# Optimization experiments

Measured on AMD Instinct MI355X. Metric: run time of the kernel, lower is better.

The kernel has to match this reference:

```python
import jax, jax.numpy as jnp
import numpy as np

B, N, D, L = 16, 100, 1024, 2000


def setup_inputs() -> dict:
    key = jax.random.key(0)
    ks = jax.random.split(key, 9)
    s = 1.0 / np.sqrt(D)
    return {
        "feature": jax.random.normal(ks[0], (B, N, D), dtype=jnp.float32),
        "graph": jax.random.randint(ks[1], (B, N, N), 0, L),
        "W0": jax.random.normal(ks[2], (D, D), dtype=jnp.float32) * s,
        "W1": jax.random.normal(ks[3], (D, D), dtype=jnp.float32) * s,
        "bias": jax.random.uniform(ks[4], (L, D), dtype=jnp.float32, minval=-s, maxval=s),
        "dp_Wa": jax.random.normal(ks[5], (D, D), dtype=jnp.float32) * s,
        "dp_ba": jax.random.normal(ks[6], (D,), dtype=jnp.float32) * s,
        "dp_Wb": jax.random.normal(ks[7], (D, D), dtype=jnp.float32) * s,
        "dp_bb": jax.random.normal(ks[8], (D,), dtype=jnp.float32) * s,
        "get_alpha": 0,
    }


def reference(feature, graph, W0, W1, bias, dp_Wa, dp_ba, dp_Wb, dp_bb, get_alpha):
    # ---- DirectedGraphConv.conv ----
    adj = (graph != 0).astype(feature.dtype)                     # [B,N,N]
    out = feature + feature @ W0.T + feature @ W1.T              # [B,N,D]
    out = out + jnp.take(bias, graph, axis=0).sum(axis=2)        # label-embedding gather+sum over neighbors
    # ---- relation_alpha: DotProduct(feature, feature) ----
    a = feature @ dp_Wa.T + dp_ba                                # [B,N,D]
    b = feature @ dp_Wb.T + dp_bb                                # [B,N,D]
    alpha = jnp.einsum('bik,bjk->bij', a, b)                     # [B,N,N]
    alpha = jnp.maximum(alpha, 0.0)                              # alpha[alpha<0]=0
    alpha = jnp.einsum('bij,bjk->bik', adj, alpha)               # bmm(adj, alpha)
    alpha = jax.nn.softmax(alpha, axis=1)                        # Softmax(dim=1)
    out = jnp.einsum('bij,bjk->bik', alpha, out)                 # bmm(alpha, output)
    if get_alpha:
        return (out, alpha)
    return out
```

## Files before the change

kernel.cpp:

```cpp
#include <hip/hip_runtime.h>
#include <stdint.h>

#define B_   16
#define N_   100
#define D_   1024
#define L_   2000
#define M_   1600

#define RCAP 24
#define ZMAX 2400
#define TC   12

typedef __bf16 bf16x8 __attribute__((ext_vector_type(8)));
typedef float  f32x4  __attribute__((ext_vector_type(4)));

__device__ __forceinline__ void gl_lds16(const __bf16* g, __bf16* l) {
    __builtin_amdgcn_global_load_lds(
        (const __attribute__((address_space(1))) void*)g,
        (__attribute__((address_space(3))) void*)l, 16, 0, 0);
}


__global__ void __launch_bounds__(256)
k_prep(const float* __restrict__ f,
       const float* __restrict__ W0, const float* __restrict__ W1,
       const float* __restrict__ Wa, const float* __restrict__ Wb,
       const float* __restrict__ bias,
       __bf16* __restrict__ fb, __bf16* __restrict__ wcat, __bf16* __restrict__ biasB) {
    int i = blockIdx.x * 256 + threadIdx.x;
    union { __bf16 h[8]; uint4 u; } pk;
    if (i < 204800) {
        long base = (long)i * 8;
        const float4* p = (const float4*)(f + base);
        float4 x = p[0], y = p[1];
        pk.h[0]=(__bf16)x.x; pk.h[1]=(__bf16)x.y; pk.h[2]=(__bf16)x.z; pk.h[3]=(__bf16)x.w;
        pk.h[4]=(__bf16)y.x; pk.h[5]=(__bf16)y.y; pk.h[6]=(__bf16)y.z; pk.h[7]=(__bf16)y.w;
        ((uint4*)fb)[i] = pk.u;
    } else if (i < 598016) {
        int j = i - 204800;
        long base = (long)j * 8;
        long seg = base >> 20;
        long off = base & ((1l << 20) - 1);
        if (seg == 0) {
            const float4* p0 = (const float4*)(W0 + off);
            const float4* p1 = (const float4*)(W1 + off);
            float4 a0 = p0[0], a1 = p0[1], b0 = p1[0], b1 = p1[1];
            pk.h[0]=(__bf16)(a0.x+b0.x); pk.h[1]=(__bf16)(a0.y+b0.y);
            pk.h[2]=(__bf16)(a0.z+b0.z); pk.h[3]=(__bf16)(a0.w+b0.w);
            pk.h[4]=(__bf16)(a1.x+b1.x); pk.h[5]=(__bf16)(a1.y+b1.y);
            pk.h[6]=(__bf16)(a1.z+b1.z); pk.h[7]=(__bf16)(a1.w+b1.w);
        } else {
            const float* src = (seg == 1) ? Wa : Wb;
            const float4* p = (const float4*)(src + off);
            float4 x = p[0], y = p[1];
            pk.h[0]=(__bf16)x.x; pk.h[1]=(__bf16)x.y; pk.h[2]=(__bf16)x.z; pk.h[3]=(__bf16)x.w;
            pk.h[4]=(__bf16)y.x; pk.h[5]=(__bf16)y.y; pk.h[6]=(__bf16)y.z; pk.h[7]=(__bf16)y.w;
        }
        ((uint4*)wcat)[j] = pk.u;
    } else {
        int j = i - 598016;
        long base = (long)j * 8;
        const float4* p = (const float4*)(bias + base);
        float4 x = p[0], y = p[1];
        pk.h[0]=(__bf16)x.x; pk.h[1]=(__bf16)x.y; pk.h[2]=(__bf16)x.z; pk.h[3]=(__bf16)x.w;
        pk.h[4]=(__bf16)y.x; pk.h[5]=(__bf16)y.y; pk.h[6]=(__bf16)y.z; pk.h[7]=(__bf16)y.w;
        ((uint4*)biasB)[j] = pk.u;
    }
}


#define BM 64
#define BN 128
#define BK 64

__global__ void __launch_bounds__(256)
k_gemm(const __bf16* __restrict__ A, const __bf16* __restrict__ Bw,
       const float* __restrict__ feat, const float* __restrict__ ba,
       const float* __restrict__ bbias,
       float* __restrict__ out0, float* __restrict__ aB, float* __restrict__ bB) {
    __shared__ __align__(16) __bf16 As[BM * BK];
    __shared__ __align__(16) __bf16 Bs[BN * BK];
    int t = threadIdx.x;
    int bm = blockIdx.x, bn = blockIdx.y;
    int lane = t & 63, wave = t >> 6;
    int wr = wave & 1, wc = wave >> 1;
    int lrow = lane & 15, quad = lane >> 4;

    f32x4 acc[2][4] = {};
    const __bf16* Ag = A  + (long)(bm * BM) * D_;
    const __bf16* Bg = Bw + (long)(bn * BN) * D_;

    for (int k0 = 0; k0 < D_; k0 += BK) {
        #pragma unroll
        for (int pi = 0; pi < 2; ++pi) {
            int p = pi * 256 + t, row = p >> 3, c = (p & 7) ^ (row & 7);
            gl_lds16(Ag + (long)row * D_ + k0 + c * 8, As + p * 8);
        }
        #pragma unroll
        for (int pi = 0; pi < 4; ++pi) {
            int p = pi * 256 + t, row = p >> 3, c = (p & 7) ^ (row & 7);
            gl_lds16(Bg + (long)row * D_ + k0 + c * 8, Bs + p * 8);
        }
        __syncthreads();
        #pragma unroll
        for (int ks = 0; ks < 2; ++ks) {
            bf16x8 af[2], bf[4];
            #pragma unroll
            for (int i = 0; i < 2; ++i) {
                int r = wr * 32 + i * 16 + lrow;
                int slot = r * 8 + (((ks << 2) | quad) ^ (r & 7));
                af[i] = *(const bf16x8*)(As + slot * 8);
            }
            #pragma unroll
            for (int j = 0; j < 4; ++j) {
                int r = wc * 64 + j * 16 + lrow;
                int slot = r * 8 + (((ks << 2) | quad) ^ (r & 7));
                bf[j] = *(const bf16x8*)(Bs + slot * 8);
            }
            #pragma unroll
            for (int i = 0; i < 2; ++i)
                #pragma unroll
                for (int j = 0; j < 4; ++j)
                    acc[i][j] = __builtin_amdgcn_mfma_f32_16x16x32_bf16(af[i], bf[j], acc[i][j], 0, 0, 0);
        }
        __syncthreads();
    }

    int nbase = bn * BN;
    int seg = nbase >> 10;
    #pragma unroll
    for (int i = 0; i < 2; ++i) {
        int gm0 = bm * BM + wr * 32 + i * 16 + quad * 4;
        #pragma unroll
        for (int j = 0; j < 4; ++j) {
            int col = (nbase + wc * 64 + j * 16 + lrow) & 1023;
            #pragma unroll
            for (int r = 0; r < 4; ++r) {
                long m = gm0 + r;
                float v = acc[i][j][r];
                if (seg == 0)      out0[m * D_ + col] = v + feat[m * D_ + col];
                else if (seg == 1) aB[m * D_ + col]   = v + ba[col];
                else               bB[m * D_ + col]   = v + bbias[col];
            }
        }
    }
}


__global__ void __launch_bounds__(256)
k_ga(const int* __restrict__ graph, const __bf16* __restrict__ biasB,
     float* __restrict__ out0, const float* __restrict__ aB,
     const float* __restrict__ bB, float* __restrict__ wl, float* __restrict__ cwG) {
    __shared__ int rowCnt[N_], rowOff[N_], rowRank[N_];
    __shared__ int ndvS, totZS;
    __shared__ int zjL[ZMAX];
    __shared__ short prL[ZMAX];
    __shared__ float corrL[RCAP][4];
    __shared__ float wred[4][4];

    int t = threadIdx.x;
    if (blockIdx.x < 1600) {
        int bi = blockIdx.x;
        if (t < N_) rowCnt[t] = graph[(long)bi * N_ + t];
        __syncthreads();
        float a0 = 0.f, a1 = 0.f, a2 = 0.f, a3 = 0.f;
        #pragma unroll 4
        for (int j = 0; j < N_; ++j) {
            int lb = rowCnt[j];
            union { uint2 u; __bf16 h[4]; } pk;
            pk.u = ((const uint2*)(biasB + (long)lb * D_))[t];
            a0 += (float)pk.h[0]; a1 += (float)pk.h[1];
            a2 += (float)pk.h[2]; a3 += (float)pk.h[3];
        }
        float4* o = (float4*)(out0 + (long)bi * D_) + t;
        float4 cur = *o;
        cur.x += a0; cur.y += a1; cur.z += a2; cur.w += a3;
        *o = cur;
        return;
    }

    int pid = blockIdx.x - 1600;
    int b = pid / 25, kc = pid - b * 25;
    int lane = t & 63, wave = t >> 6;

    const int* g = graph + (long)b * N_ * N_;
    if (t < N_) {
        int c = 0;
        for (int j = 0; j < N_; ++j) if (g[t * N_ + j] == 0) ++c;
        rowCnt[t] = c;
    }
    if (t < RCAP * 4) corrL[t >> 2][t & 3] = 0.f;
    __syncthreads();
    if (t == 0) {
        int off = 0, rank = 0;
        for (int i = 0; i < N_; ++i) {
            if (rowCnt[i] > 0 && rank < RCAP) {
                rowRank[i] = rank; rowOff[i] = off; off += rowCnt[i]; ++rank;
            } else rowRank[i] = -1;
        }
        ndvS = rank; totZS = off;
    }
    __syncthreads();
    if (t < N_ && rowRank[t] >= 0) {
        int pos = rowOff[t], r = rowRank[t];
        for (int j = 0; j < N_; ++j)
            if (g[t * N_ + j] == 0) { zjL[pos] = j; prL[pos] = (short)r; ++pos; }
    }
    __syncthreads();
    int Z = totZS, ndv = ndvS;

    int k0 = kc * 4;
    float4 bv[4];
    #pragma unroll
    for (int kk = 0; kk < 4; ++kk)
        bv[kk] = *(const float4*)(bB + ((long)(b * N_ + k0 + kk)) * D_ + t * 4);

    for (int q = 0; q < Z; ++q) {
        const float* ar = aB + ((long)(b * N_ + zjL[q])) * D_;
        float4 av = *(const float4*)(ar + t * 4);
        float s[4];
        #pragma unroll
        for (int kk = 0; kk < 4; ++kk)
            s[kk] = av.x * bv[kk].x + av.y * bv[kk].y + av.z * bv[kk].z + av.w * bv[kk].w;
        #pragma unroll
        for (int off = 32; off > 0; off >>= 1)
            #pragma unroll
            for (int kk = 0; kk < 4; ++kk) s[kk] += __shfl_xor(s[kk], off);
        if (lane == 0) { wred[wave][0]=s[0]; wred[wave][1]=s[1]; wred[wave][2]=s[2]; wred[wave][3]=s[3]; }
        __syncthreads();
        if (t < 4) {
            float v = wred[0][t] + wred[1][t] + wred[2][t] + wred[3][t];
            corrL[prL[q]][t] += fmaxf(v, 0.f);
        }
        __syncthreads();
    }

    if (t < 4) {
        int k = k0 + t;
        float denom = (float)(N_ - ndv);
        for (int r = 0; r < ndv; ++r) {
            float e = __expf(-corrL[r][t]);
            corrL[r][t] = e;
            denom += e;
        }
        float w = 1.f / denom;
        wl[b * N_ + k] = w;
        for (int r = 0; r < ndv; ++r)
            cwG[((long)b * RCAP + r) * N_ + k] = corrL[r][t] * w;
    }
}


__global__ void __launch_bounds__(256)
k_mix(const int* __restrict__ graph, const float* __restrict__ wl,
      const float* __restrict__ cwG, const float* __restrict__ out0,
      float* __restrict__ out) {
    int b = blockIdx.x, dq = blockIdx.y;
    int t = threadIdx.x, c = t & 127, h = t >> 7;
    int d0 = dq * 128;
    __shared__ int hasZ[N_], mapL[N_], ndvS;
    __shared__ float wT[TC][N_];
    __shared__ float parts[2][TC][128];

    const int* g = graph + (long)b * N_ * N_;
    if (t < N_) {
        int z = 0;
        for (int j = 0; j < N_; ++j) if (g[t * N_ + j] == 0) { z = 1; break; }
        hasZ[t] = z;
    }
    __syncthreads();
    if (t < N_) {
        int rank = 0;
        for (int i = 0; i < t; ++i) rank += hasZ[i];
        mapL[t] = (hasZ[t] && rank < RCAP) ? 1 + rank : 0;
    }
    if (t == 0) {
        int n = 0;
        for (int i = 0; i < N_; ++i) n += hasZ[i];
        ndvS = min(n, RCAP);
    }
    __syncthreads();
    int ndv = ndvS, ntask = ndv + 1;

    const float* o0 = out0 + (long)b * N_ * D_ + d0;
    for (int cb = 0; cb < ntask; cb += TC) {
        for (int idx = t; idx < TC * N_; idx += 256) {
            int rr = idx / N_, j = idx - rr * N_;
            int task = cb + rr;
            float v = 0.f;
            if (task == 0)         v = wl[b * N_ + j];
            else if (task <= ndv)  v = cwG[((long)b * RCAP + task - 1) * N_ + j];
            wT[rr][j] = v;
        }
        __syncthreads();
        float acc[TC] = {};
        #pragma unroll 2
        for (int j = h * 50; j < h * 50 + 50; ++j) {
            float v = o0[(long)j * D_ + c];
            #pragma unroll
            for (int rr = 0; rr < TC; ++rr) acc[rr] += wT[rr][j] * v;
        }
        #pragma unroll
        for (int rr = 0; rr < TC; ++rr) parts[h][rr][c] = acc[rr];
        __syncthreads();
        for (int i = h * 50; i < h * 50 + 50; ++i) {
            int task = mapL[i];
            if (task >= cb && task < cb + TC) {
                int rr = task - cb;
                out[((long)(b * N_ + i)) * D_ + d0 + c] = parts[0][rr][c] + parts[1][rr][c];
            }
        }
        __syncthreads();
    }
}


extern "C" void kernel_launch(void* const* d_in, const int* in_sizes, int n_in,
                              void* d_out, int out_size, void* d_ws, size_t ws_size,
                              hipStream_t stream) {
    const float* feature = (const float*)d_in[0];
    const int*   graph   = (const int*)d_in[1];
    const float* W0      = (const float*)d_in[2];
    const float* W1      = (const float*)d_in[3];
    const float* bias    = (const float*)d_in[4];
    const float* dp_Wa   = (const float*)d_in[5];
    const float* dp_ba   = (const float*)d_in[6];
    const float* dp_Wb   = (const float*)d_in[7];
    const float* dp_bb   = (const float*)d_in[8];
    float* out = (float*)d_out;

    char* w = (char*)d_ws;
    __bf16* fb16  = (__bf16*)(w);
    __bf16* wcat  = (__bf16*)(w + 3276800);
    __bf16* biasB = (__bf16*)(w + 9568256);
    float*  out0  = (float*)(w + 13664256);
    float*  aB    = (float*)(w + 20217856);
    float*  bB    = (float*)(w + 26771456);
    float*  wl    = (float*)(w + 33325056);
    float*  cwG   = (float*)(w + 33331456);

    k_prep<<<3336, 256, 0, stream>>>(feature, W0, W1, dp_Wa, dp_Wb, bias,
                                     fb16, wcat, biasB);
    k_gemm<<<dim3(25, 24), 256, 0, stream>>>(fb16, wcat, feature, dp_ba, dp_bb,
                                             out0, aB, bB);
    k_ga<<<2000, 256, 0, stream>>>(graph, biasB, out0, aB, bB, wl, cwG);
    k_mix<<<dim3(B_, 8), 256, 0, stream>>>(graph, wl, cwG, out0, out);
}
```

Before: 186.0 us.

## Replace bias gather-sum with histogram-count GEMM on MFMA and widen mix kernel

The per-row gather of label embeddings summed over neighbours becomes a dense product. Each row first builds a label histogram (counts stored as bf16), and that count matrix is multiplied by a transposed bf16 bias matrix padded to K=2048 using MFMA tiles. This replaces 1600 blocks of scattered bias-row reads with 200 GEMM blocks, at the cost of extra prep work for the transpose and histogram plus about 6.5MB of count writes. Separately, the mix kernel now processes float4 vectors with four partial sums and half as many blocks.

After: 178.6 us. -4.0%, faster.

```diff
diff --git a/kernel.cpp b/kernel.cpp
--- a/kernel.cpp
+++ b/kernel.cpp
@@ -6,6 +6,7 @@
 #define D_   1024
 #define L_   2000
 #define M_   1600
+#define KP   2048
 
 #define RCAP 24
 #define ZMAX 2400
@@ -25,46 +26,66 @@
 k_prep(const float* __restrict__ f,
        const float* __restrict__ W0, const float* __restrict__ W1,
        const float* __restrict__ Wa, const float* __restrict__ Wb,
-       const float* __restrict__ bias,
-       __bf16* __restrict__ fb, __bf16* __restrict__ wcat, __bf16* __restrict__ biasB) {
-    int i = blockIdx.x * 256 + threadIdx.x;
-    union { __bf16 h[8]; uint4 u; } pk;
-    if (i < 204800) {
-        long base = (long)i * 8;
-        const float4* p = (const float4*)(f + base);
-        float4 x = p[0], y = p[1];
-        pk.h[0]=(__bf16)x.x; pk.h[1]=(__bf16)x.y; pk.h[2]=(__bf16)x.z; pk.h[3]=(__bf16)x.w;
-        pk.h[4]=(__bf16)y.x; pk.h[5]=(__bf16)y.y; pk.h[6]=(__bf16)y.z; pk.h[7]=(__bf16)y.w;
-        ((uint4*)fb)[i] = pk.u;
-    } else if (i < 598016) {
-        int j = i - 204800;
-        long base = (long)j * 8;
-        long seg = base >> 20;
-        long off = base & ((1l << 20) - 1);
-        if (seg == 0) {
-            const float4* p0 = (const float4*)(W0 + off);
-            const float4* p1 = (const float4*)(W1 + off);
-            float4 a0 = p0[0], a1 = p0[1], b0 = p1[0], b1 = p1[1];
-            pk.h[0]=(__bf16)(a0.x+b0.x); pk.h[1]=(__bf16)(a0.y+b0.y);
-            pk.h[2]=(__bf16)(a0.z+b0.z); pk.h[3]=(__bf16)(a0.w+b0.w);
-            pk.h[4]=(__bf16)(a1.x+b1.x); pk.h[5]=(__bf16)(a1.y+b1.y);
-            pk.h[6]=(__bf16)(a1.z+b1.z); pk.h[7]=(__bf16)(a1.w+b1.w);
-        } else {
-            const float* src = (seg == 1) ? Wa : Wb;
-            const float4* p = (const float4*)(src + off);
+       const float* __restrict__ bias, const int* __restrict__ graph,
+       __bf16* __restrict__ fb, __bf16* __restrict__ wcat,
+       __bf16* __restrict__ biasBT, __bf16* __restrict__ cnt) {
+    int bid = blockIdx.x, t = threadIdx.x;
+    __shared__ float lds[32][33];
+    __shared__ unsigned int hist[KP];
+
+    if (bid < 2336) {
+        int i = bid * 256 + t;
+        union { __bf16 h[8]; uint4 u; } pk;
+        if (i < 204800) {
+            long base = (long)i * 8;
+            const float4* p = (const float4*)(f + base);
             float4 x = p[0], y = p[1];
             pk.h[0]=(__bf16)x.x; pk.h[1]=(__bf16)x.y; pk.h[2]=(__bf16)x.z; pk.h[3]=(__bf16)x.w;
             pk.h[4]=(__bf16)y.x; pk.h[5]=(__bf16)y.y; pk.h[6]=(__bf16)y.z; pk.h[7]=(__bf16)y.w;
-        }
-        ((uint4*)wcat)[j] = pk.u;
+            ((uint4*)fb)[i] = pk.u;
+        } else {
+            int j = i - 204800;
+            long base = (long)j * 8;
+            long seg = base >> 20;
+            long off = base & ((1l << 20) - 1);
+            if (seg == 0) {
+                const float4* p0 = (const float4*)(W0 + off);
+                const float4* p1 = (const float4*)(W1 + off);
+                float4 a0 = p0[0], a1 = p0[1], b0 = p1[0], b1 = p1[1];
+                pk.h[0]=(__bf16)(a0.x+b0.x); pk.h[1]=(__bf16)(a0.y+b0.y);
+                pk.h[2]=(__bf16)(a0.z+b0.z); pk.h[3]=(__bf16)(a0.w+b0.w);
+                pk.h[4]=(__bf16)(a1.x+b1.x); pk.h[5]=(__bf16)(a1.y+b1.y);
+                pk.h[6]=(__bf16)(a1.z+b1.z); pk.h[7]=(__bf16)(a1.w+b1.w);
+            } else {
+                const float* src = (seg == 1) ? Wa : Wb;
+                const float4* p = (const float4*)(src + off);
+                float4 x = p[0], y = p[1];
+                pk.h[0]=(__bf16)x.x; pk.h[1]=(__bf16)x.y; pk.h[2]=(__bf16)x.z; pk.h[3]=(__bf16)x.w;
+                pk.h[4]=(__bf16)y.x; pk.h[5]=(__bf16)y.y; pk.h[6]=(__bf16)y.z; pk.h[7]=(__bf16)y.w;
+            }
+            ((uint4*)wcat)[j] = pk.u;
+        }
+    } else if (bid < 4384) {
+        int tb = bid - 2336;
+        int lt = tb >> 5, dt = tb & 31;
+        int l0 = lt * 32, d0 = dt * 32;
+        int r = t >> 3, cq = (t & 7) * 4;
+        float4 v = make_float4(0.f, 0.f, 0.f, 0.f);
+        if (l0 + r < L_) v = *(const float4*)(bias + (long)(l0 + r) * D_ + d0 + cq);
+        lds[r][cq]=v.x; lds[r][cq+1]=v.y; lds[r][cq+2]=v.z; lds[r][cq+3]=v.w;
+        __syncthreads();
+        union { __bf16 h[4]; uint2 u; } pk;
+        #pragma unroll
+        for (int q = 0; q < 4; ++q) pk.h[q] = (__bf16)lds[cq + q][r];
+        *(uint2*)(biasBT + (long)(d0 + r) * KP + l0 + cq) = pk.u;
     } else {
-        int j = i - 598016;
-        long base = (long)j * 8;
-        const float4* p = (const float4*)(bias + base);
-        float4 x = p[0], y = p[1];
-        pk.h[0]=(__bf16)x.x; pk.h[1]=(__bf16)x.y; pk.h[2]=(__bf16)x.z; pk.h[3]=(__bf16)x.w;
-        pk.h[4]=(__bf16)y.x; pk.h[5]=(__bf16)y.y; pk.h[6]=(__bf16)y.z; pk.h[7]=(__bf16)y.w;
-        ((uint4*)biasB)[j] = pk.u;
+        int m = bid - 4384;
+        for (int k = t; k < KP; k += 256) hist[k] = 0u;
+        __syncthreads();
+        if (t < N_) atomicAdd(&hist[graph[(long)m * N_ + t]], 1u);
+        __syncthreads();
+        for (int k = t; k < KP; k += 256)
+            cnt[(long)m * KP + k] = (__bf16)(float)hist[k];
     }
 }
 
@@ -148,9 +169,76 @@
 
 
 __global__ void __launch_bounds__(256)
-k_ga(const int* __restrict__ graph, const __bf16* __restrict__ biasB,
-     float* __restrict__ out0, const float* __restrict__ aB,
-     const float* __restrict__ bB, float* __restrict__ wl, float* __restrict__ cwG) {
+k_post1(const int* __restrict__ graph, const __bf16* __restrict__ cnt,
+        const __bf16* __restrict__ biasBT, const float* __restrict__ aB,
+        const float* __restrict__ bB, float* __restrict__ out0,
+        float* __restrict__ wl, float* __restrict__ cwG) {
+    int t = threadIdx.x;
+
+    if (blockIdx.x < 200) {
+        __shared__ __align__(16) __bf16 As[BM * BK];
+        __shared__ __align__(16) __bf16 Bs[BN * BK];
+        int bm = blockIdx.x >> 3, bn = blockIdx.x & 7;
+        int lane = t & 63, wave = t >> 6;
+        int wr = wave & 1, wc = wave >> 1;
+        int lrow = lane & 15, quad = lane >> 4;
+
+        f32x4 acc[2][4] = {};
+        const __bf16* Ag = cnt    + (long)(bm * BM) * KP;
+        const __bf16* Bg = biasBT + (long)(bn * BN) * KP;
+
+        for (int k0 = 0; k0 < KP; k0 += BK) {
+            #pragma unroll
+            for (int pi = 0; pi < 2; ++pi) {
+                int p = pi * 256 + t, row = p >> 3, c = (p & 7) ^ (row & 7);
+                gl_lds16(Ag + (long)row * KP + k0 + c * 8, As + p * 8);
+            }
+            #pragma unroll
+            for (int pi = 0; pi < 4; ++pi) {
+                int p = pi * 256 + t, row = p >> 3, c = (p & 7) ^ (row & 7);
+                gl_lds16(Bg + (long)row * KP + k0 + c * 8, Bs + p * 8);
+            }
+            __syncthreads();
+            #pragma unroll
+            for (int ks = 0; ks < 2; ++ks) {
+                bf16x8 af[2], bf[4];
+                #pragma unroll
+                for (int i = 0; i < 2; ++i) {
+                    int r = wr * 32 + i * 16 + lrow;
+                    int slot = r * 8 + (((ks << 2) | quad) ^ (r & 7));
+                    af[i] = *(const bf16x8*)(As + slot * 8);
+                }
+                #pragma unroll
+                for (int j = 0; j < 4; ++j) {
+                    int r = wc * 64 + j * 16 + lrow;
+                    int slot = r * 8 + (((ks << 2) | quad) ^ (r & 7));
+                    bf[j] = *(const bf16x8*)(Bs + slot * 8);
+                }
+                #pragma unroll
+                for (int i = 0; i < 2; ++i)
+                    #pragma unroll
+                    for (int j = 0; j < 4; ++j)
+                        acc[i][j] = __builtin_amdgcn_mfma_f32_16x16x32_bf16(af[i], bf[j], acc[i][j], 0, 0, 0);
+            }
+            __syncthreads();
+        }
+
+        #pragma unroll
+        for (int i = 0; i < 2; ++i) {
+            int gm0 = bm * BM + wr * 32 + i * 16 + quad * 4;
+            #pragma unroll
+            for (int j = 0; j < 4; ++j) {
+                int col = bn * BN + wc * 64 + j * 16 + lrow;
+                #pragma unroll
+                for (int r = 0; r < 4; ++r) {
+                    long m = gm0 + r;
+                    out0[m * D_ + col] += acc[i][j][r];
+                }
+            }
+        }
+        return;
+    }
+
     __shared__ int rowCnt[N_], rowOff[N_], rowRank[N_];
     __shared__ int ndvS, totZS;
     __shared__ int zjL[ZMAX];
@@ -158,28 +246,7 @@
     __shared__ float corrL[RCAP][4];
     __shared__ float wred[4][4];
 
-    int t = threadIdx.x;
-    if (blockIdx.x < 1600) {
-        int bi = blockIdx.x;
-        if (t < N_) rowCnt[t] = graph[(long)bi * N_ + t];
-        __syncthreads();
-        float a0 = 0.f, a1 = 0.f, a2 = 0.f, a3 = 0.f;
-        #pragma unroll 4
-        for (int j = 0; j < N_; ++j) {
-            int lb = rowCnt[j];
-            union { uint2 u; __bf16 h[4]; } pk;
-            pk.u = ((const uint2*)(biasB + (long)lb * D_))[t];
-            a0 += (float)pk.h[0]; a1 += (float)pk.h[1];
-            a2 += (float)pk.h[2]; a3 += (float)pk.h[3];
-        }
-        float4* o = (float4*)(out0 + (long)bi * D_) + t;
-        float4 cur = *o;
-        cur.x += a0; cur.y += a1; cur.z += a2; cur.w += a3;
-        *o = cur;
-        return;
-    }
-
-    int pid = blockIdx.x - 1600;
+    int pid = blockIdx.x - 200;
     int b = pid / 25, kc = pid - b * 25;
     int lane = t & 63, wave = t >> 6;
 
@@ -256,11 +323,11 @@
       const float* __restrict__ cwG, const float* __restrict__ out0,
       float* __restrict__ out) {
     int b = blockIdx.x, dq = blockIdx.y;
-    int t = threadIdx.x, c = t & 127, h = t >> 7;
-    int d0 = dq * 128;
+    int t = threadIdx.x, c4 = t & 63, q = t >> 6;
+    int d0 = dq * 256;
     __shared__ int hasZ[N_], mapL[N_], ndvS;
     __shared__ float wT[TC][N_];
-    __shared__ float parts[2][TC][128];
+    __shared__ f32x4 parts[4][TC][64];
 
     const int* g = graph + (long)b * N_ * N_;
     if (t < N_) {
@@ -293,21 +360,22 @@
             wT[rr][j] = v;
         }
         __syncthreads();
-        float acc[TC] = {};
-        #pragma unroll 2
-        for (int j = h * 50; j < h * 50 + 50; ++j) {
-            float v = o0[(long)j * D_ + c];
+        f32x4 acc[TC] = {};
+        for (int j = q * 25; j < q * 25 + 25; ++j) {
+            f32x4 v = *(const f32x4*)(o0 + (long)j * D_ + c4 * 4);
             #pragma unroll
             for (int rr = 0; rr < TC; ++rr) acc[rr] += wT[rr][j] * v;
         }
         #pragma unroll
-        for (int rr = 0; rr < TC; ++rr) parts[h][rr][c] = acc[rr];
-        __syncthreads();
-        for (int i = h * 50; i < h * 50 + 50; ++i) {
+        for (int rr = 0; rr < TC; ++rr) parts[q][rr][c4] = acc[rr];
+        __syncthreads();
+        for (int i = q * 25; i < q * 25 + 25; ++i) {
             int task = mapL[i];
             if (task >= cb && task < cb + TC) {
                 int rr = task - cb;
-                out[((long)(b * N_ + i)) * D_ + d0 + c] = parts[0][rr][c] + parts[1][rr][c];
+                f32x4 s = parts[0][rr][c4] + parts[1][rr][c4]
+                        + parts[2][rr][c4] + parts[3][rr][c4];
+                *(f32x4*)(out + ((long)(b * N_ + i)) * D_ + d0 + c4 * 4) = s;
             }
         }
         __syncthreads();
@@ -330,19 +398,20 @@
     float* out = (float*)d_out;
 
     char* w = (char*)d_ws;
-    __bf16* fb16  = (__bf16*)(w);
-    __bf16* wcat  = (__bf16*)(w + 3276800);
-    __bf16* biasB = (__bf16*)(w + 9568256);
-    float*  out0  = (float*)(w + 13664256);
-    float*  aB    = (float*)(w + 20217856);
-    float*  bB    = (float*)(w + 26771456);
-    float*  wl    = (float*)(w + 33325056);
-    float*  cwG   = (float*)(w + 33331456);
-
-    k_prep<<<3336, 256, 0, stream>>>(feature, W0, W1, dp_Wa, dp_Wb, bias,
-                                     fb16, wcat, biasB);
+    __bf16* fb16   = (__bf16*)(w);
+    __bf16* wcat   = (__bf16*)(w + 3276800);
+    __bf16* cnt    = (__bf16*)(w + 9568256);
+    __bf16* biasBT = (__bf16*)(w + 16121856);
+    float*  out0   = (float*)(w + 20316160);
+    float*  aB     = (float*)(w + 26869760);
+    float*  bB     = (float*)(w + 33423360);
+    float*  wl     = (float*)(w + 39976960);
+    float*  cwG    = (float*)(w + 39983360);
+
+    k_prep<<<5984, 256, 0, stream>>>(feature, W0, W1, dp_Wa, dp_Wb, bias, graph,
+                                     fb16, wcat, biasBT, cnt);
     k_gemm<<<dim3(25, 24), 256, 0, stream>>>(fb16, wcat, feature, dp_ba, dp_bb,
                                              out0, aB, bB);
-    k_ga<<<2000, 256, 0, stream>>>(graph, biasB, out0, aB, bB, wl, cwG);
-    k_mix<<<dim3(B_, 8), 256, 0, stream>>>(graph, wl, cwG, out0, out);
-}
+    k_post1<<<600, 256, 0, stream>>>(graph, cnt, biasBT, aB, bB, out0, wl, cwG);
+    k_mix<<<dim3(B_, 4), 256, 0, stream>>>(graph, wl, cwG, out0, out);
+}
```
